# Kernel tuning notes

Hardware: AMD Instinct MI355X
Metric: run time of the kernel (lower is better)

## Reference

```python
import jax, jax.numpy as jnp
import numpy as np

NEG_SLOPE = 0.2
LN_EPS = 1e-5


def setup_inputs() -> dict:
    key = jax.random.key(0)
    k1, k2, k3, k4 = jax.random.split(key, 4)
    N, K, F, O = 100000, 16, 128, 128
    face_features = jax.random.normal(k1, (N, F), dtype=jnp.float32)
    adjacency = jax.random.randint(k2, (N, K), 0, N, dtype=jnp.int64)
    # Linear(2F -> O) params (torch layout: W [O, 2F])
    W = jax.random.normal(k3, (O, 2 * F), dtype=jnp.float32) / np.sqrt(2 * F)
    b = jnp.zeros((O,), dtype=jnp.float32)
    gamma = jnp.ones((O,), dtype=jnp.float32)
    beta = jnp.zeros((O,), dtype=jnp.float32)
    return {"face_features": face_features, "adjacency": adjacency,
            "W": W, "b": b, "gamma": gamma, "beta": beta}


def reference(face_features, adjacency, W, b, gamma, beta):
    # mask for valid neighbors (-1 = padding)
    mask = (adjacency != -1).astype(face_features.dtype)[..., None]  # [N, K, 1]
    neigh = face_features[jnp.clip(adjacency, 0, None)]              # [N, K, F]
    denom = jnp.clip(mask.sum(axis=1), 1.0, None)                    # [N, 1]
    mean_neigh = (neigh * mask).sum(axis=1) / denom                  # [N, F]
    x = jnp.concatenate([face_features, mean_neigh], axis=1)         # [N, 2F]
    h = x @ W.T + b                                                  # [N, O]
    mu = h.mean(axis=-1, keepdims=True)
    var = ((h - mu) ** 2).mean(axis=-1, keepdims=True)
    h = (h - mu) / jnp.sqrt(var + LN_EPS) * gamma + beta
    return jnp.where(h >= 0, h, NEG_SLOPE * h)
```

## Files before the change

### kernel.cpp

```cpp
#include <hip/hip_runtime.h>
#include <stdint.h>

#define F 128
#define KNB 16
#define TWO_F 256
#define ROWS 64
#define THREADS 256
#define XSTRIDE 264
#define HSTR 133
#define LN_EPS 1e-5f
#define NEG_SLOPE 0.2f

typedef unsigned short u16;
typedef __bf16 bf16x8 __attribute__((ext_vector_type(8)));
typedef float f32x4 __attribute__((ext_vector_type(4)));

union BF8 { bf16x8 v; u16 us[8]; uint4 u4; };

__device__ __forceinline__ float b2f(u16 u) {
    union { float f; uint32_t i; } v; v.i = ((uint32_t)u) << 16; return v.f;
}
__device__ __forceinline__ u16 f2b(float f) {
    union { float f; uint32_t i; } v; v.f = f;
    uint32_t r = (v.i + 0x7FFFu + ((v.i >> 16) & 1u)) >> 16;
    return (u16)r;
}

extern "C" __global__ void cast_f32_bf16(const float* __restrict__ src,
                                         u16* __restrict__ dst, int n8) {
    const int i = blockIdx.x * blockDim.x + threadIdx.x;
    if (i >= n8) return;
    const float4* s = (const float4*)src + (size_t)i * 2;
    const float4 a = s[0], b = s[1];
    BF8 o;
    o.us[0] = f2b(a.x); o.us[1] = f2b(a.y); o.us[2] = f2b(a.z); o.us[3] = f2b(a.w);
    o.us[4] = f2b(b.x); o.us[5] = f2b(b.y); o.us[6] = f2b(b.z); o.us[7] = f2b(b.w);
    ((uint4*)dst)[i] = o.u4;
}

template <int MODE>
__global__ __launch_bounds__(THREADS, 4)
void gnn_fused(const float* __restrict__ feat_f32, const u16* __restrict__ feat_bf,
               const int* __restrict__ adj,
               const float* __restrict__ W_f32, const u16* __restrict__ W_bf,
               const float* __restrict__ bias, const float* __restrict__ gamma,
               const float* __restrict__ beta,
               float* __restrict__ out, int N)
{
    __shared__ __align__(16) char smem[ROWS * XSTRIDE * 2 + ROWS * KNB * 4];
    u16* xs   = (u16*)smem;
    int* adjs = (int*)(smem + ROWS * XSTRIDE * 2);
    float* hb = (float*)smem;

    const int tid = threadIdx.x;
    const long block0 = (long)blockIdx.x * ROWS;

    {
        const int flat = tid * 4;
        const long base = block0 * KNB + flat;
        const long total = (long)N * KNB;
        if (base + 3 < total) {
            *(int4*)(adjs + flat) = *(const int4*)(adj + base);
        } else {
            for (int j = 0; j < 4; ++j)
                adjs[flat + j] = (base + j < total) ? (int)adj[base + j] : -1;
        }
    }
    __syncthreads();

    {
        const int r  = tid >> 2;
        const int q4 = tid & 3;
        const long rg = block0 + r;
        const int fbase = q4 * 32;
        u16* xrow = xs + r * XSTRIDE;

        if (rg < N) {
            if (MODE == 2) {
                const uint4* src = (const uint4*)(feat_bf + rg * F + fbase);
                uint4* dst = (uint4*)(xrow + fbase);
                #pragma unroll
                for (int j = 0; j < 4; ++j) dst[j] = src[j];
            } else {
                const float4* s = (const float4*)(feat_f32 + rg * F + fbase);
                uint4* dst = (uint4*)(xrow + fbase);
                #pragma unroll
                for (int j = 0; j < 4; ++j) {
                    const float4 a = s[j * 2], b = s[j * 2 + 1];
                    BF8 o;
                    o.us[0] = f2b(a.x); o.us[1] = f2b(a.y); o.us[2] = f2b(a.z); o.us[3] = f2b(a.w);
                    o.us[4] = f2b(b.x); o.us[5] = f2b(b.y); o.us[6] = f2b(b.z); o.us[7] = f2b(b.w);
                    dst[j] = o.u4;
                }
            }

            float acc[32];
            #pragma unroll
            for (int t = 0; t < 32; ++t) acc[t] = 0.f;
            int cnt = 0;
            for (int k = 0; k < KNB; ++k) {
                const int idx = adjs[r * KNB + k];
                if (idx >= 0 && idx < N) {
                    ++cnt;
                    if (MODE == 2) {
                        const uint4* ns = (const uint4*)(feat_bf + (long)idx * F + fbase);
                        #pragma unroll
                        for (int j = 0; j < 4; ++j) {
                            BF8 u; u.u4 = ns[j];
                            #pragma unroll
                            for (int t = 0; t < 8; ++t) acc[j * 8 + t] += b2f(u.us[t]);
                        }
                    } else {
                        const float4* ns = (const float4*)(feat_f32 + (long)idx * F + fbase);
                        #pragma unroll
                        for (int j = 0; j < 8; ++j) {
                            const float4 a = ns[j];
                            acc[j * 4 + 0] += a.x; acc[j * 4 + 1] += a.y;
                            acc[j * 4 + 2] += a.z; acc[j * 4 + 3] += a.w;
                        }
                    }
                }
            }
            const float scale = 1.f / (float)(cnt > 0 ? cnt : 1);
            uint4* mdst = (uint4*)(xrow + F + fbase);
            #pragma unroll
            for (int j = 0; j < 4; ++j) {
                BF8 o;
                #pragma unroll
                for (int t = 0; t < 8; ++t) o.us[t] = f2b(acc[j * 8 + t] * scale);
                mdst[j] = o.u4;
            }
        } else {
            const uint4 z = make_uint4(0, 0, 0, 0);
            uint4* d0 = (uint4*)(xrow + fbase);
            uint4* d1 = (uint4*)(xrow + F + fbase);
            #pragma unroll
            for (int j = 0; j < 4; ++j) { d0[j] = z; d1[j] = z; }
        }
    }
    __syncthreads();

    const int wave = tid >> 6;
    const int lane = tid & 63;
    const int ln15 = lane & 15;
    const int quad = lane >> 4;
    const int rb   = wave * 16;

    f32x4 accf[8];
    #pragma unroll
    for (int c = 0; c < 8; ++c) accf[c] = (f32x4){0.f, 0.f, 0.f, 0.f};

    const u16* arow = xs + (rb + ln15) * XSTRIDE + quad * 8;

    #pragma unroll
    for (int ks = 0; ks < 8; ++ks) {
        const bf16x8 afrag = *(const bf16x8*)(arow + ks * 32);
        #pragma unroll
        for (int c = 0; c < 8; ++c) {
            bf16x8 bfrag;
            if (MODE >= 1) {
                bfrag = *(const bf16x8*)(W_bf + (size_t)(c * 16 + ln15) * TWO_F + quad * 8 + ks * 32);
            } else {
                const float* wr = W_f32 + (size_t)(c * 16 + ln15) * TWO_F + quad * 8 + ks * 32;
                const float4 a = *(const float4*)wr, b = *(const float4*)(wr + 4);
                BF8 o;
                o.us[0] = f2b(a.x); o.us[1] = f2b(a.y); o.us[2] = f2b(a.z); o.us[3] = f2b(a.w);
                o.us[4] = f2b(b.x); o.us[5] = f2b(b.y); o.us[6] = f2b(b.z); o.us[7] = f2b(b.w);
                bfrag = o.v;
            }
            accf[c] = __builtin_amdgcn_mfma_f32_16x16x32_bf16(afrag, bfrag, accf[c], 0, 0, 0);
        }
    }

    float bval[8];
    #pragma unroll
    for (int c = 0; c < 8; ++c) bval[c] = bias[c * 16 + ln15];

    __syncthreads();

    #pragma unroll
    for (int c = 0; c < 8; ++c) {
        #pragma unroll
        for (int t = 0; t < 4; ++t) {
            const int rr = quad * 4 + t;
            hb[(rb + rr) * HSTR + c * 16 + ln15] = accf[c][t] + bval[c];
        }
    }
    __syncthreads();

    const int er = lane >> 2;
    const int eq = lane & 3;
    const float* hr = hb + (rb + er) * HSTR + eq * 32;
    float sum = 0.f, sq = 0.f;
    #pragma unroll
    for (int t = 0; t < 32; ++t) { const float v = hr[t]; sum += v; sq += v * v; }
    sum += __shfl_xor(sum, 1); sq += __shfl_xor(sq, 1);
    sum += __shfl_xor(sum, 2); sq += __shfl_xor(sq, 2);

    const float mu   = sum * (1.f / 128.f);
    const float var  = sq * (1.f / 128.f) - mu * mu;
    const float rsig = rsqrtf(fmaxf(var, 0.f) + LN_EPS);

    const long org = block0 + rb + er;
    if (org < N) {
        const int cb = eq * 32;
        float* orow = out + org * F + cb;
        #pragma unroll
        for (int j = 0; j < 8; ++j) {
            const float4 g  = *(const float4*)(gamma + cb + j * 4);
            const float4 bt = *(const float4*)(beta  + cb + j * 4);
            float4 o;
            o.x = (hr[j * 4 + 0] - mu) * rsig * g.x + bt.x;
            o.y = (hr[j * 4 + 1] - mu) * rsig * g.y + bt.y;
            o.z = (hr[j * 4 + 2] - mu) * rsig * g.z + bt.z;
            o.w = (hr[j * 4 + 3] - mu) * rsig * g.w + bt.w;
            o.x = (o.x >= 0.f) ? o.x : NEG_SLOPE * o.x;
            o.y = (o.y >= 0.f) ? o.y : NEG_SLOPE * o.y;
            o.z = (o.z >= 0.f) ? o.z : NEG_SLOPE * o.z;
            o.w = (o.w >= 0.f) ? o.w : NEG_SLOPE * o.w;
            *(float4*)(orow + j * 4) = o;
        }
    }
}

extern "C" void kernel_launch(void* const* d_in, const int* in_sizes, int n_in,
                              void* d_out, int out_size, void* d_ws, size_t ws_size,
                              hipStream_t stream) {
    const float* feat  = (const float*)d_in[0];
    const int*   adj   = (const int*)d_in[1];
    const float* W     = (const float*)d_in[2];
    const float* bias  = (const float*)d_in[3];
    const float* gamma = (const float*)d_in[4];
    const float* beta  = (const float*)d_in[5];
    float* out = (float*)d_out;

    const int N = in_sizes[0] / F;
    const size_t needW = (size_t)TWO_F * F * sizeof(u16);
    const size_t needF = (size_t)N * F * sizeof(u16);
    u16* wsW = (u16*)d_ws;
    u16* wsF = (u16*)((char*)d_ws + needW);

    const int mode = (ws_size >= needW + needF) ? 2 : (ws_size >= needW ? 1 : 0);

    if (mode >= 1) {
        const int n8 = TWO_F * F / 8;
        cast_f32_bf16<<<dim3((n8 + 255) / 256), dim3(256), 0, stream>>>(W, wsW, n8);
    }
    if (mode == 2) {
        const int n8 = N * F / 8;
        cast_f32_bf16<<<dim3((n8 + 255) / 256), dim3(256), 0, stream>>>(feat, wsF, n8);
    }

    const int blocks = (N + ROWS - 1) / ROWS;
    if (mode == 2) {
        gnn_fused<2><<<dim3(blocks), dim3(THREADS), 0, stream>>>(feat, wsF, adj, W, wsW, bias, gamma, beta, out, N);
    } else if (mode == 1) {
        gnn_fused<1><<<dim3(blocks), dim3(THREADS), 0, stream>>>(feat, wsF, adj, W, wsW, bias, gamma, beta, out, N);
    } else {
        gnn_fused<0><<<dim3(blocks), dim3(THREADS), 0, stream>>>(feat, wsF, adj, W, wsW, bias, gamma, beta, out, N);
    }
}
```

Before: 223.4 us.

## Gather neighbor features directly into MFMA A-fragments, dropping LDS staging

Each lane now gathers and averages neighbor features for the exact row and k-slice it feeds into the MFMA, so the A operand is built in registers instead of being staged through shared memory. This removes the LDS tile for x and adjacency and two block barriers. In exchange, each thread handles one row with 16 lanes spread across features, so the gathered loads become 16-byte strided chunks (quad*8 + j*32) rather than contiguous 64-byte spans. Register pressure also rises from holding 8 A-fragments.

```diff
diff --git a/kernel.cpp b/kernel.cpp
--- a/kernel.cpp
+++ b/kernel.cpp
@@ -6,7 +6,6 @@
 #define TWO_F 256
 #define ROWS 64
 #define THREADS 256
-#define XSTRIDE 264
 #define HSTR 133
 #define LN_EPS 1e-5f
 #define NEG_SLOPE 0.2f
@@ -38,7 +37,7 @@
     ((uint4*)dst)[i] = o.u4;
 }
 
-template <int MODE>
+template <int FEAT_BF, int W_BF>
 __global__ __launch_bounds__(THREADS, 4)
 void gnn_fused(const float* __restrict__ feat_f32, const u16* __restrict__ feat_bf,
                const int* __restrict__ adj,
@@ -47,136 +46,108 @@
                const float* __restrict__ beta,
                float* __restrict__ out, int N)
 {
-    __shared__ __align__(16) char smem[ROWS * XSTRIDE * 2 + ROWS * KNB * 4];
-    u16* xs   = (u16*)smem;
-    int* adjs = (int*)(smem + ROWS * XSTRIDE * 2);
-    float* hb = (float*)smem;
-
-    const int tid = threadIdx.x;
-    const long block0 = (long)blockIdx.x * ROWS;
-
-    {
-        const int flat = tid * 4;
-        const long base = block0 * KNB + flat;
-        const long total = (long)N * KNB;
-        if (base + 3 < total) {
-            *(int4*)(adjs + flat) = *(const int4*)(adj + base);
-        } else {
-            for (int j = 0; j < 4; ++j)
-                adjs[flat + j] = (base + j < total) ? (int)adj[base + j] : -1;
-        }
-    }
-    __syncthreads();
-
-    {
-        const int r  = tid >> 2;
-        const int q4 = tid & 3;
-        const long rg = block0 + r;
-        const int fbase = q4 * 32;
-        u16* xrow = xs + r * XSTRIDE;
-
-        if (rg < N) {
-            if (MODE == 2) {
-                const uint4* src = (const uint4*)(feat_bf + rg * F + fbase);
-                uint4* dst = (uint4*)(xrow + fbase);
-                #pragma unroll
-                for (int j = 0; j < 4; ++j) dst[j] = src[j];
-            } else {
-                const float4* s = (const float4*)(feat_f32 + rg * F + fbase);
-                uint4* dst = (uint4*)(xrow + fbase);
-                #pragma unroll
-                for (int j = 0; j < 4; ++j) {
-                    const float4 a = s[j * 2], b = s[j * 2 + 1];
-                    BF8 o;
-                    o.us[0] = f2b(a.x); o.us[1] = f2b(a.y); o.us[2] = f2b(a.z); o.us[3] = f2b(a.w);
-                    o.us[4] = f2b(b.x); o.us[5] = f2b(b.y); o.us[6] = f2b(b.z); o.us[7] = f2b(b.w);
-                    dst[j] = o.u4;
-                }
-            }
-
-            float acc[32];
-            #pragma unroll
-            for (int t = 0; t < 32; ++t) acc[t] = 0.f;
-            int cnt = 0;
-            for (int k = 0; k < KNB; ++k) {
-                const int idx = adjs[r * KNB + k];
-                if (idx >= 0 && idx < N) {
-                    ++cnt;
-                    if (MODE == 2) {
-                        const uint4* ns = (const uint4*)(feat_bf + (long)idx * F + fbase);
-                        #pragma unroll
-                        for (int j = 0; j < 4; ++j) {
-                            BF8 u; u.u4 = ns[j];
-                            #pragma unroll
-                            for (int t = 0; t < 8; ++t) acc[j * 8 + t] += b2f(u.us[t]);
-                        }
-                    } else {
-                        const float4* ns = (const float4*)(feat_f32 + (long)idx * F + fbase);
-                        #pragma unroll
-                        for (int j = 0; j < 8; ++j) {
-                            const float4 a = ns[j];
-                            acc[j * 4 + 0] += a.x; acc[j * 4 + 1] += a.y;
-                            acc[j * 4 + 2] += a.z; acc[j * 4 + 3] += a.w;
-                        }
-                    }
-                }
-            }
-            const float scale = 1.f / (float)(cnt > 0 ? cnt : 1);
-            uint4* mdst = (uint4*)(xrow + F + fbase);
-            #pragma unroll
-            for (int j = 0; j < 4; ++j) {
-                BF8 o;
-                #pragma unroll
-                for (int t = 0; t < 8; ++t) o.us[t] = f2b(acc[j * 8 + t] * scale);
-                mdst[j] = o.u4;
-            }
-        } else {
-            const uint4 z = make_uint4(0, 0, 0, 0);
-            uint4* d0 = (uint4*)(xrow + fbase);
-            uint4* d1 = (uint4*)(xrow + F + fbase);
-            #pragma unroll
-            for (int j = 0; j < 4; ++j) { d0[j] = z; d1[j] = z; }
-        }
-    }
-    __syncthreads();
-
+    __shared__ float hb[ROWS * HSTR];
+
+    const int tid  = threadIdx.x;
     const int wave = tid >> 6;
     const int lane = tid & 63;
     const int ln15 = lane & 15;
     const int quad = lane >> 4;
+    const int fb   = quad * 8;
     const int rb   = wave * 16;
 
+    const long rowA  = (long)blockIdx.x * ROWS + rb + ln15;
+    const bool rok   = rowA < (long)N;
+    const long rsafe = rok ? rowA : 0;
+
+    float acc[32];
+    #pragma unroll
+    for (int t = 0; t < 32; ++t) acc[t] = 0.f;
+    int cnt = 0;
+
+    if (rok) {
+        const int* adjr = adj + rowA * KNB;
+        for (int k = 0; k < KNB; ++k) {
+            const int idx = adjr[k];
+            if (idx >= 0 && idx < N) {
+                ++cnt;
+                if (FEAT_BF) {
+                    const u16* nb = feat_bf + (size_t)idx * F + fb;
+                    #pragma unroll
+                    for (int j = 0; j < 4; ++j) {
+                        BF8 u; u.u4 = *(const uint4*)(nb + j * 32);
+                        #pragma unroll
+                        for (int t = 0; t < 8; ++t) acc[j * 8 + t] += b2f(u.us[t]);
+                    }
+                } else {
+                    const float* nb = feat_f32 + (size_t)idx * F + fb;
+                    #pragma unroll
+                    for (int j = 0; j < 4; ++j) {
+                        const float4 p0 = *(const float4*)(nb + j * 32);
+                        const float4 p1 = *(const float4*)(nb + j * 32 + 4);
+                        acc[j * 8 + 0] += p0.x; acc[j * 8 + 1] += p0.y;
+                        acc[j * 8 + 2] += p0.z; acc[j * 8 + 3] += p0.w;
+                        acc[j * 8 + 4] += p1.x; acc[j * 8 + 5] += p1.y;
+                        acc[j * 8 + 6] += p1.z; acc[j * 8 + 7] += p1.w;
+                    }
+                }
+            }
+        }
+    }
+    const float scale = 1.f / (float)(cnt > 0 ? cnt : 1);
+
+    bf16x8 afrag[8];
+    if (FEAT_BF) {
+        const u16* orow = feat_bf + rsafe * F + fb;
+        #pragma unroll
+        for (int j = 0; j < 4; ++j)
+            afrag[j] = *(const bf16x8*)(orow + j * 32);
+    } else {
+        const float* orow = feat_f32 + rsafe * F + fb;
+        #pragma unroll
+        for (int j = 0; j < 4; ++j) {
+            const float4 p0 = *(const float4*)(orow + j * 32);
+            const float4 p1 = *(const float4*)(orow + j * 32 + 4);
+            BF8 o;
+            o.us[0] = f2b(p0.x); o.us[1] = f2b(p0.y); o.us[2] = f2b(p0.z); o.us[3] = f2b(p0.w);
+            o.us[4] = f2b(p1.x); o.us[5] = f2b(p1.y); o.us[6] = f2b(p1.z); o.us[7] = f2b(p1.w);
+            afrag[j] = o.v;
+        }
+    }
+    #pragma unroll
+    for (int j = 0; j < 4; ++j) {
+        BF8 o;
+        #pragma unroll
+        for (int t = 0; t < 8; ++t) o.us[t] = f2b(acc[j * 8 + t] * scale);
+        afrag[4 + j] = o.v;
+    }
+
     f32x4 accf[8];
     #pragma unroll
     for (int c = 0; c < 8; ++c) accf[c] = (f32x4){0.f, 0.f, 0.f, 0.f};
 
-    const u16* arow = xs + (rb + ln15) * XSTRIDE + quad * 8;
-
     #pragma unroll
     for (int ks = 0; ks < 8; ++ks) {
-        const bf16x8 afrag = *(const bf16x8*)(arow + ks * 32);
         #pragma unroll
         for (int c = 0; c < 8; ++c) {
             bf16x8 bfrag;
-            if (MODE >= 1) {
-                bfrag = *(const bf16x8*)(W_bf + (size_t)(c * 16 + ln15) * TWO_F + quad * 8 + ks * 32);
+            if (W_BF) {
+                bfrag = *(const bf16x8*)(W_bf + (size_t)(c * 16 + ln15) * TWO_F + fb + ks * 32);
             } else {
-                const float* wr = W_f32 + (size_t)(c * 16 + ln15) * TWO_F + quad * 8 + ks * 32;
+                const float* wr = W_f32 + (size_t)(c * 16 + ln15) * TWO_F + fb + ks * 32;
                 const float4 a = *(const float4*)wr, b = *(const float4*)(wr + 4);
                 BF8 o;
                 o.us[0] = f2b(a.x); o.us[1] = f2b(a.y); o.us[2] = f2b(a.z); o.us[3] = f2b(a.w);
                 o.us[4] = f2b(b.x); o.us[5] = f2b(b.y); o.us[6] = f2b(b.z); o.us[7] = f2b(b.w);
                 bfrag = o.v;
             }
-            accf[c] = __builtin_amdgcn_mfma_f32_16x16x32_bf16(afrag, bfrag, accf[c], 0, 0, 0);
+            accf[c] = __builtin_amdgcn_mfma_f32_16x16x32_bf16(afrag[ks], bfrag, accf[c], 0, 0, 0);
         }
     }
 
     float bval[8];
     #pragma unroll
     for (int c = 0; c < 8; ++c) bval[c] = bias[c * 16 + ln15];
-
-    __syncthreads();
 
     #pragma unroll
     for (int c = 0; c < 8; ++c) {
@@ -201,7 +172,7 @@
     const float var  = sq * (1.f / 128.f) - mu * mu;
     const float rsig = rsqrtf(fmaxf(var, 0.f) + LN_EPS);
 
-    const long org = block0 + rb + er;
+    const long org = (long)blockIdx.x * ROWS + rb + er;
     if (org < N) {
         const int cb = eq * 32;
         float* orow = out + org * F + cb;
@@ -253,10 +224,10 @@
 
     const int blocks = (N + ROWS - 1) / ROWS;
     if (mode == 2) {
-        gnn_fused<2><<<dim3(blocks), dim3(THREADS), 0, stream>>>(feat, wsF, adj, W, wsW, bias, gamma, beta, out, N);
+        gnn_fused<1, 1><<<dim3(blocks), dim3(THREADS), 0, stream>>>(feat, wsF, adj, W, wsW, bias, gamma, beta, out, N);
     } else if (mode == 1) {
-        gnn_fused<1><<<dim3(blocks), dim3(THREADS), 0, stream>>>(feat, wsF, adj, W, wsW, bias, gamma, beta, out, N);
+        gnn_fused<0, 1><<<dim3(blocks), dim3(THREADS), 0, stream>>>(feat, wsF, adj, W, wsW, bias, gamma, beta, out, N);
     } else {
-        gnn_fused<0><<<dim3(blocks), dim3(THREADS), 0, stream>>>(feat, wsF, adj, W, wsW, bias, gamma, beta, out, N);
-    }
-}
+        gnn_fused<0, 0><<<dim3(blocks), dim3(THREADS), 0, stream>>>(feat, wsF, adj, W, wsW, bias, gamma, beta, out, N);
+    }
+}
```

New measurement: 247.0 us. +10.5%, slower.
